# Optimization experiments

Hardware: AMD Instinct MI355X
Metric: run time of the kernel (lower is better)

The kernel has to match this reference:

```python
import jax, jax.numpy as jnp
import numpy as np

RX = (2, 9)
RY = (4, 9)
G, O = 64, 2          # column chunk size and overlap (hardcoded in original forward)
GK = RX[1]            # Gaussian (uniform box) kernel size, must be odd
M = N = 512


def _patches(x, kh, kw, pc, pr):
    # torch: F.pad(x,(pr,pr,pc,pc)).unfold(-2,kh,1).unfold(-2,kw,1).flatten(-2)
    xp = jnp.pad(x, ((0, 0), (0, 0), (pc, pc), (pr, pr)))
    p = jax.lax.conv_general_dilated_patches(xp, (kh, kw), (1, 1), 'VALID')  # (b, kh*kw, m, n) since c==1
    return jnp.moveaxis(p, 1, -1)[:, None]  # (b,1,m,n,kh*kw)


def _spatial_kernel(kh, kw):
    d = (jnp.arange(kh, dtype=jnp.float32) - kh // 2)[:, None] ** 2 \
        + (jnp.arange(kw, dtype=jnp.float32) - kw // 2)[None, :] ** 2
    return jnp.exp(-d.reshape(-1) / ((kh * kw) / 4.0) ** 2)


def _gen_weight(ych, kh, kw, pc, pr, sigma):
    p = _patches(ych, kh, kw, pc, pr)
    w = jnp.exp(-((p - ych[..., None]) ** 2) / (sigma / 2.0) ** 2)  # range (bilateral) term
    w = w * _spatial_kernel(kh, kw)                                  # spatial Gaussian term
    w = w * _patches(jnp.ones_like(ych), kh, kw, pc, pr)             # zero out padded taps
    return w / w.sum(-1, keepdims=True)


def _boxfilter(x, weight, kh, kw, pc, pr):
    return (_patches(x, kh, kw, pc, pr) * weight).sum(-1)


def _forward(X, y, r):
    sigma = r[0] * (y.max() - y.min())
    kh0, kw0, pc0, pr0 = 2 * RX[0] + 1, 2 * RY[0] + 1, RX[0], RY[0]  # detail kernel
    kh1, kw1, pc1, pr1 = 2 * RX[1] + 1, 2 * RY[1] + 1, RX[1], RY[1]  # base kernel
    gk = jnp.ones((1, 1, GK, GK), X.dtype) / float(GK * GK)
    pad = GK // 2
    conv = lambda z: jax.lax.conv_general_dilated(z, gk, (1, 1), [(pad, pad), (pad, pad)])

    # Angle = [0]: rotate(.,0,expand=True) and CenterCrop(m,n) are identities.
    XX, yy = X, y
    XXbase, yybase = conv(XX), conv(yy)
    XXdetail, yydetail = XX - XXbase, yy - yybase

    n = X.shape[-1]
    idx = np.arange(n)
    chunks = [idx[i:i + G] for i in range(0, n, G - O)]
    if len(chunks[-1]) <= 5:
        chunks[-2] = np.arange(chunks[-2][0], n)
        del chunks[-1]

    bdetail, Abase, bbase = [], [], []
    for index, ck in enumerate(chunks):
        s, e = int(ck[0]), int(ck[-1]) + 1
        Xb, Xd = XXbase[..., s:e], XXdetail[..., s:e]
        yb, yd = yybase[..., s:e], yydetail[..., s:e]
        wD = _gen_weight(Xd, kh0, kw0, pc0, pr0, sigma)
        wB = _gen_weight(Xb, kh1, kw1, pc1, pr1, sigma)
        lo = 0 if index == 0 else O // 2
        hi = None if index == len(chunks) - 1 else -(O // 2)
        bdetail.append(_boxfilter(yd - Xd, wD, kh0, kw0, pc0, pr0)[..., lo:hi])
        mean_y = _boxfilter(yb, wB, kh1, kw1, pc1, pr1)
        mean_x = _boxfilter(Xb, wB, kh1, kw1, pc1, pr1)
        var_x = _boxfilter(Xb * Xb, wB, kh1, kw1, pc1, pr1) - mean_x * mean_x
        cov_xy = _boxfilter(Xb * yb, wB, kh1, kw1, pc1, pr1) - mean_x * mean_y
        A = cov_xy / (var_x + 1e-6)
        b = mean_y - A * mean_x
        bbase.append(b[..., lo:hi])
        Abase.append(A[..., lo:hi])

    bdetail = jnp.concatenate(bdetail, -1)
    Abase = jnp.concatenate(Abase, -1)
    bbase = jnp.concatenate(bbase, -1)
    return Abase * XXbase + bbase + XXdetail + bdetail


def setup_inputs() -> dict:
    key = jax.random.key(0)
    k1, k2, k3 = jax.random.split(key, 3)
    X = jax.random.uniform(k1, (1, 1, M, N), dtype=jnp.float32)
    y = jax.random.uniform(k2, (1, 1, M, N), dtype=jnp.float32)
    r = jax.random.uniform(k3, (1,), dtype=jnp.float32)
    return {"X": X, "y": y, "r": r}


def reference(X, y, r):
    return _forward(X, y, r)
```

## Files before the change

kernel.cpp:

```cpp
#include <hip/hip_runtime.h>

#define W 512

__device__ __forceinline__ float fexp2(float x) {
#if __has_builtin(__builtin_amdgcn_exp2f)
    return __builtin_amdgcn_exp2f(x);
#else
    return __expf(x * 0.6931471805599453f);
#endif
}

__global__ __launch_bounds__(256) void k_minmax(const float* __restrict__ y,
                                                float2* __restrict__ partial) {
    __shared__ float smn[256], smx[256];
    int t = threadIdx.x;
    const float4* y4 = (const float4*)y;
    float4 v = y4[blockIdx.x * 256 + t];
    float mn = fminf(fminf(v.x, v.y), fminf(v.z, v.w));
    float mx = fmaxf(fmaxf(v.x, v.y), fmaxf(v.z, v.w));
    smn[t] = mn; smx[t] = mx;
    __syncthreads();
    for (int off = 128; off > 0; off >>= 1) {
        if (t < off) {
            smn[t] = fminf(smn[t], smn[t + off]);
            smx[t] = fmaxf(smx[t], smx[t + off]);
        }
        __syncthreads();
    }
    if (t == 0) partial[blockIdx.x] = make_float2(smn[0], smx[0]);
}

__global__ __launch_bounds__(256) void k_box(const float* __restrict__ X,
                                             const float* __restrict__ y,
                                             const float2* __restrict__ partial,
                                             const float* __restrict__ r,
                                             float2* __restrict__ bXY_g,
                                             float2* __restrict__ dXD_g,
                                             float* __restrict__ k2out) {
    __shared__ __align__(16) float lds[1920];
    float* sX  = lds;
    float* sY  = sX + 576;
    float* csX = sY + 576;
    float* csY = csX + 384;

    int tx = threadIdx.x, ty = threadIdx.y;
    int t = ty * 16 + tx;
    int c0 = blockIdx.x * 16, r0 = blockIdx.y * 16;

    if (blockIdx.x == 0 && blockIdx.y == 0) {
        float2* red = (float2*)lds;
        red[t] = partial[t];
        __syncthreads();
        for (int off = 128; off > 0; off >>= 1) {
            if (t < off) {
                red[t].x = fminf(red[t].x, red[t + off].x);
                red[t].y = fmaxf(red[t].y, red[t + off].y);
            }
            __syncthreads();
        }
        if (t == 0) {
            float sigma = r[0] * (red[0].y - red[0].x);
            float hh = 0.5f * sigma;
            k2out[0] = -1.4426950408889634f / (hh * hh);
        }
        __syncthreads();
    }

    for (int i = t; i < 576; i += 256) {
        int rr = i / 24, cc = i - rr * 24;
        int gr = r0 - 4 + rr, gc = c0 - 4 + cc;
        bool ok = ((unsigned)gr < 512u) & ((unsigned)gc < 512u);
        float xv = 0.f, yv = 0.f;
        if (ok) { xv = X[gr * W + gc]; yv = y[gr * W + gc]; }
        sX[i] = xv; sY[i] = yv;
    }
    __syncthreads();

    for (int i = t; i < 384; i += 256) {
        int rr = i / 24, cc = i - rr * 24;
        float ax = 0.f, ay = 0.f;
#pragma unroll
        for (int k = 0; k < 9; ++k) { ax += sX[(rr + k) * 24 + cc]; ay += sY[(rr + k) * 24 + cc]; }
        csX[i] = ax; csY[i] = ay;
    }
    __syncthreads();

    const float inv81 = 1.0f / 81.0f;
    float ax = 0.f, ay = 0.f;
#pragma unroll
    for (int k = 0; k < 9; ++k) { ax += csX[ty * 24 + tx + k]; ay += csY[ty * 24 + tx + k]; }
    float Xb = ax * inv81, yb = ay * inv81;
    float xc = sX[(ty + 4) * 24 + tx + 4];
    float yc = sY[(ty + 4) * 24 + tx + 4];
    float xd = xc - Xb;
    int p = (r0 + ty) * W + (c0 + tx);
    bXY_g[p] = make_float2(Xb, yb);
    dXD_g[p] = make_float2(xd, (yc - yb) - xd);
}

__global__ __launch_bounds__(256, 4) void k_bil(const float2* __restrict__ bXY_g,
                                                const float2* __restrict__ dXD_g,
                                                const float* __restrict__ k2buf,
                                                float* __restrict__ out) {
    __shared__ float sbx[19];
    __shared__ float sdy[5];
    __shared__ __align__(16) float2 bXYs[34 * 34];
    __shared__ __align__(16) float2 dXDs[20 * 24];

    int tx = threadIdx.x, ty = threadIdx.y;
    int t = ty * 16 + tx;
    int c0 = blockIdx.x * 16, r0 = blockIdx.y * 16;

    if (t < 19)      { int d = t - 9;  sbx[t]      = __expf(-(float)(d * d) / 8145.0625f); }
    else if (t < 24) { int d = t - 21; sdy[t - 19] = __expf(-(float)(d * d) / 126.5625f); }

    float k2 = k2buf[0];

    for (int i = t; i < 34 * 34; i += 256) {
        int rr = i / 34, cc2 = i - rr * 34;
        int gr = r0 - 9 + rr, gc = c0 - 9 + cc2;
        float2 v = make_float2(0.f, 0.f);
        if (((unsigned)gr < 512u) & ((unsigned)gc < 512u)) v = bXY_g[gr * W + gc];
        bXYs[i] = v;
    }
    for (int i = t; i < 20 * 24; i += 256) {
        int rr = i / 24, cc2 = i - rr * 24;
        int gr = r0 - 2 + rr, gc = c0 - 4 + cc2;
        float2 v = make_float2(0.f, 0.f);
        if (((unsigned)gr < 512u) & ((unsigned)gc < 512u)) v = dXD_g[gr * W + gc];
        dXDs[i] = v;
    }
    __syncthreads();

    int c = c0 + tx;
    int h = r0 + ty;

    int chunk = (c == 0) ? 0 : (c - 1) / 62;
    if (chunk > 8) chunk = 8;
    int s = 62 * chunk;
    int e = (chunk == 8) ? 512 : (s + 64);

    const float ksb = -1.4426950408889634f / 8145.0625f;
    const float ksd = -1.4426950408889634f / 126.5625f;
    float cc[19];
#pragma unroll
    for (int j = 0; j < 19; ++j) {
        int nc = c - 9 + j, d = j - 9;
        cc[j] = ((nc >= s) & (nc < e)) ? ksb * (float)(d * d) : -1e30f;
    }
    float ccd[9];
#pragma unroll
    for (int j = 0; j < 9; ++j) {
        int nc = c - 4 + j, d = j - 4;
        ccd[j] = ((nc >= s) & (nc < e)) ? ksd * (float)(d * d) : -1e30f;
    }

    float Xc = bXYs[(ty + 9) * 34 + tx + 9].x;
    float Xd = dXDs[(ty + 2) * 24 + tx + 4].x;

    float sw = 0.f, swx = 0.f, swy = 0.f, swxx = 0.f, swxy = 0.f;
#pragma unroll 1
    for (int k = 0; k < 19; ++k) {
        int nh = h - 9 + k;
        if ((unsigned)nh >= 512u) continue;
        const float2* xr = (const float2*)bXYs + (ty + k) * 34 + tx;
        float rs = 0.f, rsx = 0.f, rsy = 0.f, rsxx = 0.f, rsxy = 0.f;
#pragma unroll
        for (int j = 0; j < 19; ++j) {
            float2 v = xr[j];
            float u = v.x - Xc;
            float a = fmaf(u * k2, u, cc[j]);
            float w = fexp2(a);
            rs += w;
            rsx = fmaf(w, v.x, rsx);
            rsy = fmaf(w, v.y, rsy);
            float tt = w * v.x;
            rsxx = fmaf(tt, v.x, rsxx);
            rsxy = fmaf(tt, v.y, rsxy);
        }
        float ey = sbx[k];
        sw   = fmaf(ey, rs,   sw);
        swx  = fmaf(ey, rsx,  swx);
        swy  = fmaf(ey, rsy,  swy);
        swxx = fmaf(ey, rsxx, swxx);
        swxy = fmaf(ey, rsxy, swxy);
    }

    float swd = 0.f, sv = 0.f;
#pragma unroll 1
    for (int k = 0; k < 5; ++k) {
        int nh = h - 2 + k;
        if ((unsigned)nh >= 512u) continue;
        const float2* dr2 = (const float2*)dXDs + (ty + k) * 24 + tx;
        float rs = 0.f, rv = 0.f;
#pragma unroll
        for (int j = 0; j < 9; ++j) {
            float2 v = dr2[j];
            float u = v.x - Xd;
            float a = fmaf(u * k2, u, ccd[j]);
            float w = fexp2(a);
            rs += w;
            rv = fmaf(w, v.y, rv);
        }
        swd = fmaf(sdy[k], rs, swd);
        sv  = fmaf(sdy[k], rv, sv);
    }

    float inv  = 1.0f / sw;
    float mx   = swx * inv, my = swy * inv;
    float varx = fmaf(-mx, mx, swxx * inv);
    float cov  = fmaf(-mx, my, swxy * inv);
    float A    = cov / (varx + 1e-6f);
    float b    = my - A * mx;
    float bd   = sv / swd;
    out[h * W + c] = fmaf(A, Xc, b) + Xd + bd;
}

__global__ __launch_bounds__(256, 4) void k_fused(const float* __restrict__ X,
                                                  const float* __restrict__ y,
                                                  const float2* __restrict__ partial,
                                                  const float* __restrict__ r,
                                                  float* __restrict__ out) {
    __shared__ float sbx[19];
    __shared__ float sdy[5];
    __shared__ __align__(16) char ldsbuf[38624];
    float*  sX  = (float*)ldsbuf;
    float*  sY  = sX + 42 * 42;
    float*  csX = sY + 42 * 42;
    float*  csY = csX + 34 * 42;
    float2* bXY = (float2*)(csY + 34 * 42);
    float2* dXD = bXY + 34 * 34;
    float2* red = (float2*)sX;

    int tx = threadIdx.x, ty = threadIdx.y;
    int t = ty * 16 + tx;
    int c0 = blockIdx.x * 16, r0 = blockIdx.y * 16;

    if (t < 19)      { int d = t - 9;  sbx[t]      = __expf(-(float)(d * d) / 8145.0625f); }
    else if (t < 24) { int d = t - 21; sdy[t - 19] = __expf(-(float)(d * d) / 126.5625f); }

    red[t] = partial[t];
    __syncthreads();
    for (int off = 128; off > 0; off >>= 1) {
        if (t < off) {
            red[t].x = fminf(red[t].x, red[t + off].x);
            red[t].y = fmaxf(red[t].y, red[t + off].y);
        }
        __syncthreads();
    }
    float2 mm0 = red[0];
    __syncthreads();
    float sigma = r[0] * (mm0.y - mm0.x);
    float hh = 0.5f * sigma;
    float k2 = -1.4426950408889634f / (hh * hh);

    for (int i = t; i < 42 * 42; i += 256) {
        int rr = i / 42, cc2 = i - rr * 42;
        int gr = r0 - 13 + rr, gc = c0 - 13 + cc2;
        bool ok = ((unsigned)gr < 512u) & ((unsigned)gc < 512u);
        float xv = 0.f, yv = 0.f;
        if (ok) { xv = X[gr * W + gc]; yv = y[gr * W + gc]; }
        sX[i] = xv; sY[i] = yv;
    }
    __syncthreads();

    for (int i = t; i < 34 * 42; i += 256) {
        int rr = i / 42, cc2 = i - rr * 42;
        float ax = 0.f, ay = 0.f;
#pragma unroll
        for (int k = 0; k < 9; ++k) { ax += sX[(rr + k) * 42 + cc2]; ay += sY[(rr + k) * 42 + cc2]; }
        csX[i] = ax; csY[i] = ay;
    }
    __syncthreads();

    const float inv81 = 1.0f / 81.0f;
    for (int i = t; i < 34 * 34; i += 256) {
        int rr = i / 34, cc2 = i - rr * 34;
        float ax = 0.f, ay = 0.f;
#pragma unroll
        for (int k = 0; k < 9; ++k) { ax += csX[rr * 42 + cc2 + k]; ay += csY[rr * 42 + cc2 + k]; }
        bXY[i] = make_float2(ax * inv81, ay * inv81);
    }
    __syncthreads();

    for (int i = t; i < 20 * 24; i += 256) {
        int rr = i / 24, cc2 = i - rr * 24;
        float2 b2 = bXY[(rr + 7) * 34 + (cc2 + 5)];
        float xc = sX[(rr + 11) * 42 + (cc2 + 9)];
        float yc = sY[(rr + 11) * 42 + (cc2 + 9)];
        float xd = xc - b2.x;
        dXD[i] = make_float2(xd, (yc - b2.y) - xd);
    }
    __syncthreads();

    int c = c0 + tx;
    int h = r0 + ty;
    int chunk = (c == 0) ? 0 : (c - 1) / 62;
    if (chunk > 8) chunk = 8;
    int s = 62 * chunk;
    int e = (chunk == 8) ? 512 : (s + 64);

    const float ksb = -1.4426950408889634f / 8145.0625f;
    const float ksd = -1.4426950408889634f / 126.5625f;
    float cc[19];
#pragma unroll
    for (int j = 0; j < 19; ++j) {
        int nc = c - 9 + j, d = j - 9;
        cc[j] = ((nc >= s) & (nc < e)) ? ksb * (float)(d * d) : -1e30f;
    }
    float ccd[9];
#pragma unroll
    for (int j = 0; j < 9; ++j) {
        int nc = c - 4 + j, d = j - 4;
        ccd[j] = ((nc >= s) & (nc < e)) ? ksd * (float)(d * d) : -1e30f;
    }

    float Xc = bXY[(ty + 9) * 34 + tx + 9].x;
    float Xd = dXD[(ty + 2) * 24 + tx + 4].x;

    float sw = 0.f, swx = 0.f, swy = 0.f, swxx = 0.f, swxy = 0.f;
#pragma unroll 1
    for (int k = 0; k < 19; ++k) {
        int nh = h - 9 + k;
        if ((unsigned)nh >= 512u) continue;
        const float2* xr = bXY + (ty + k) * 34 + tx;
        float rs = 0.f, rsx = 0.f, rsy = 0.f, rsxx = 0.f, rsxy = 0.f;
#pragma unroll
        for (int j = 0; j < 19; ++j) {
            float2 v = xr[j];
            float u = v.x - Xc;
            float a = fmaf(u * k2, u, cc[j]);
            float w = fexp2(a);
            rs += w;
            rsx = fmaf(w, v.x, rsx);
            rsy = fmaf(w, v.y, rsy);
            float tt = w * v.x;
            rsxx = fmaf(tt, v.x, rsxx);
            rsxy = fmaf(tt, v.y, rsxy);
        }
        float ey = sbx[k];
        sw   = fmaf(ey, rs,   sw);
        swx  = fmaf(ey, rsx,  swx);
        swy  = fmaf(ey, rsy,  swy);
        swxx = fmaf(ey, rsxx, swxx);
        swxy = fmaf(ey, rsxy, swxy);
    }

    float swd = 0.f, sv = 0.f;
#pragma unroll 1
    for (int k = 0; k < 5; ++k) {
        int nh = h - 2 + k;
        if ((unsigned)nh >= 512u) continue;
        const float2* dr2 = dXD + (ty + k) * 24 + tx;
        float rs = 0.f, rv = 0.f;
#pragma unroll
        for (int j = 0; j < 9; ++j) {
            float2 v = dr2[j];
            float u = v.x - Xd;
            float a = fmaf(u * k2, u, ccd[j]);
            float w = fexp2(a);
            rs += w;
            rv = fmaf(w, v.y, rv);
        }
        swd = fmaf(sdy[k], rs, swd);
        sv  = fmaf(sdy[k], rv, sv);
    }

    float inv  = 1.0f / sw;
    float mx   = swx * inv, my = swy * inv;
    float varx = fmaf(-mx, mx, swxx * inv);
    float cov  = fmaf(-mx, my, swxy * inv);
    float A    = cov / (varx + 1e-6f);
    float b    = my - A * mx;
    float bd   = sv / swd;
    out[h * W + c] = fmaf(A, Xc, b) + Xd + bd;
}

extern "C" void kernel_launch(void* const* d_in, const int* in_sizes, int n_in,
                              void* d_out, int out_size, void* d_ws, size_t ws_size,
                              hipStream_t stream) {
    const float* X = (const float*)d_in[0];
    const float* y = (const float*)d_in[1];
    const float* r = (const float*)d_in[2];
    float* out = (float*)d_out;

    float2* partial = (float2*)d_ws;
    float*  k2buf   = (float*)((char*)d_ws + 2048);
    float2* bXY_g   = (float2*)((char*)d_ws + 4096);
    float2* dXD_g   = (float2*)((char*)d_ws + 4096 + 512 * 512 * 8);
    size_t need = 4096 + (size_t)2 * 512 * 512 * 8;

    k_minmax<<<256, 256, 0, stream>>>(y, partial);
    if (ws_size >= need) {
        k_box<<<dim3(32, 32), dim3(16, 16), 0, stream>>>(X, y, partial, r, bXY_g, dXD_g, k2buf);
        k_bil<<<dim3(32, 32), dim3(16, 16), 0, stream>>>(bXY_g, dXD_g, k2buf, out);
    } else {
        k_fused<<<dim3(32, 32), dim3(16, 16), 0, stream>>>(X, y, partial, r, out);
    }
}
```

Measured before the change: 96.23 us.

## Register-block bilateral kernel over four output rows per thread with 64x8 tiles

The bilateral kernel now computes four vertically adjacent output pixels per thread. Each shared-memory row of neighbours is loaded into registers once and reused across the four outputs, using shifted row-weight tables padded with zeros. Tiles change to 64 columns by 8 rows with 128-thread blocks, which cuts redundant halo loads and LDS reads per output. In exchange register pressure rises sharply (dozens of accumulators plus 38 cached values), occupancy drops, and there are fewer blocks in total (512).

```diff
diff --git a/kernel.cpp b/kernel.cpp
--- a/kernel.cpp
+++ b/kernel.cpp
@@ -98,33 +98,34 @@
     dXD_g[p] = make_float2(xd, (yc - yb) - xd);
 }
 
-__global__ __launch_bounds__(256, 4) void k_bil(const float2* __restrict__ bXY_g,
+__global__ __launch_bounds__(128, 1) void k_bil(const float2* __restrict__ bXY_g,
                                                 const float2* __restrict__ dXD_g,
                                                 const float* __restrict__ k2buf,
                                                 float* __restrict__ out) {
-    __shared__ float sbx[19];
-    __shared__ float sdy[5];
-    __shared__ __align__(16) float2 bXYs[34 * 34];
-    __shared__ __align__(16) float2 dXDs[20 * 24];
-
-    int tx = threadIdx.x, ty = threadIdx.y;
-    int t = ty * 16 + tx;
-    int c0 = blockIdx.x * 16, r0 = blockIdx.y * 16;
-
-    if (t < 19)      { int d = t - 9;  sbx[t]      = __expf(-(float)(d * d) / 8145.0625f); }
-    else if (t < 24) { int d = t - 21; sdy[t - 19] = __expf(-(float)(d * d) / 126.5625f); }
+    __shared__ float sbe[25];
+    __shared__ float sde[11];
+    __shared__ __align__(16) float2 bXYs[26 * 82];
+    __shared__ __align__(16) float2 dXDs[12 * 72];
+
+    int tx = threadIdx.x;
+    int ty = threadIdx.y;
+    int t = ty * 64 + tx;
+    int c0 = blockIdx.x * 64, r0 = blockIdx.y * 8;
+
+    if (t < 25)                 { int dy = t - 12; sbe[t] = (dy * dy <= 81) ? __expf(-(float)(dy * dy) / 8145.0625f) : 0.f; }
+    else if (t >= 32 && t < 43) { int i = t - 32; int dy = i - 5; sde[i] = (dy * dy <= 4) ? __expf(-(float)(dy * dy) / 126.5625f) : 0.f; }
 
     float k2 = k2buf[0];
 
-    for (int i = t; i < 34 * 34; i += 256) {
-        int rr = i / 34, cc2 = i - rr * 34;
+    for (int i = t; i < 26 * 82; i += 128) {
+        int rr = i / 82, cc2 = i - rr * 82;
         int gr = r0 - 9 + rr, gc = c0 - 9 + cc2;
         float2 v = make_float2(0.f, 0.f);
         if (((unsigned)gr < 512u) & ((unsigned)gc < 512u)) v = bXY_g[gr * W + gc];
         bXYs[i] = v;
     }
-    for (int i = t; i < 20 * 24; i += 256) {
-        int rr = i / 24, cc2 = i - rr * 24;
+    for (int i = t; i < 12 * 72; i += 128) {
+        int rr = i / 72, cc2 = i - rr * 72;
         int gr = r0 - 2 + rr, gc = c0 - 4 + cc2;
         float2 v = make_float2(0.f, 0.f);
         if (((unsigned)gr < 512u) & ((unsigned)gc < 512u)) v = dXD_g[gr * W + gc];
@@ -133,7 +134,7 @@
     __syncthreads();
 
     int c = c0 + tx;
-    int h = r0 + ty;
+    int h0 = r0 + 4 * ty;
 
     int chunk = (c == 0) ? 0 : (c - 1) / 62;
     if (chunk > 8) chunk = 8;
@@ -155,65 +156,98 @@
         ccd[j] = ((nc >= s) & (nc < e)) ? ksd * (float)(d * d) : -1e30f;
     }
 
-    float Xc = bXYs[(ty + 9) * 34 + tx + 9].x;
-    float Xd = dXDs[(ty + 2) * 24 + tx + 4].x;
-
-    float sw = 0.f, swx = 0.f, swy = 0.f, swxx = 0.f, swxy = 0.f;
+    float Xc[4], Xd[4];
+#pragma unroll
+    for (int p = 0; p < 4; ++p) {
+        Xc[p] = bXYs[(4 * ty + 9 + p) * 82 + tx + 9].x;
+        Xd[p] = dXDs[(4 * ty + 2 + p) * 72 + tx + 4].x;
+    }
+
+    float s_w[4], s_wx[4], s_wy[4], s_wxx[4], s_wxy[4];
+#pragma unroll
+    for (int p = 0; p < 4; ++p) { s_w[p] = 0.f; s_wx[p] = 0.f; s_wy[p] = 0.f; s_wxx[p] = 0.f; s_wxy[p] = 0.f; }
+
 #pragma unroll 1
-    for (int k = 0; k < 19; ++k) {
-        int nh = h - 9 + k;
-        if ((unsigned)nh >= 512u) continue;
-        const float2* xr = (const float2*)bXYs + (ty + k) * 34 + tx;
-        float rs = 0.f, rsx = 0.f, rsy = 0.f, rsxx = 0.f, rsxy = 0.f;
+    for (int k = 0; k < 22; ++k) {
+        int nh = h0 - 9 + k;
+        bool valid = (unsigned)nh < 512u;
+        const float2* xr = bXYs + (4 * ty + k) * 82 + tx;
+        float vx[19], vy[19];
+#pragma unroll
+        for (int j = 0; j < 19; ++j) { float2 v = xr[j]; vx[j] = v.x; vy[j] = v.y; }
+        float rs[4], rsx[4], rsy[4], rsxx[4], rsxy[4];
+#pragma unroll
+        for (int p = 0; p < 4; ++p) { rs[p] = 0.f; rsx[p] = 0.f; rsy[p] = 0.f; rsxx[p] = 0.f; rsxy[p] = 0.f; }
 #pragma unroll
         for (int j = 0; j < 19; ++j) {
-            float2 v = xr[j];
-            float u = v.x - Xc;
-            float a = fmaf(u * k2, u, cc[j]);
-            float w = fexp2(a);
-            rs += w;
-            rsx = fmaf(w, v.x, rsx);
-            rsy = fmaf(w, v.y, rsy);
-            float tt = w * v.x;
-            rsxx = fmaf(tt, v.x, rsxx);
-            rsxy = fmaf(tt, v.y, rsxy);
-        }
-        float ey = sbx[k];
-        sw   = fmaf(ey, rs,   sw);
-        swx  = fmaf(ey, rsx,  swx);
-        swy  = fmaf(ey, rsy,  swy);
-        swxx = fmaf(ey, rsxx, swxx);
-        swxy = fmaf(ey, rsxy, swxy);
-    }
-
-    float swd = 0.f, sv = 0.f;
+#pragma unroll
+            for (int p = 0; p < 4; ++p) {
+                float u = vx[j] - Xc[p];
+                float a = fmaf(u * k2, u, cc[j]);
+                float w = fexp2(a);
+                rs[p] += w;
+                rsx[p] = fmaf(w, vx[j], rsx[p]);
+                rsy[p] = fmaf(w, vy[j], rsy[p]);
+                float tt = w * vx[j];
+                rsxx[p] = fmaf(tt, vx[j], rsxx[p]);
+                rsxy[p] = fmaf(tt, vy[j], rsxy[p]);
+            }
+        }
+#pragma unroll
+        for (int p = 0; p < 4; ++p) {
+            float ey = valid ? sbe[k + 3 - p] : 0.f;
+            s_w[p]   = fmaf(ey, rs[p],   s_w[p]);
+            s_wx[p]  = fmaf(ey, rsx[p],  s_wx[p]);
+            s_wy[p]  = fmaf(ey, rsy[p],  s_wy[p]);
+            s_wxx[p] = fmaf(ey, rsxx[p], s_wxx[p]);
+            s_wxy[p] = fmaf(ey, rsxy[p], s_wxy[p]);
+        }
+    }
+
+    float s_wd[4], s_v[4];
+#pragma unroll
+    for (int p = 0; p < 4; ++p) { s_wd[p] = 0.f; s_v[p] = 0.f; }
 #pragma unroll 1
-    for (int k = 0; k < 5; ++k) {
-        int nh = h - 2 + k;
-        if ((unsigned)nh >= 512u) continue;
-        const float2* dr2 = (const float2*)dXDs + (ty + k) * 24 + tx;
-        float rs = 0.f, rv = 0.f;
+    for (int kd = 0; kd < 8; ++kd) {
+        int nh = h0 - 2 + kd;
+        bool valid = (unsigned)nh < 512u;
+        const float2* dr = dXDs + (4 * ty + kd) * 72 + tx;
+        float vx[9], vd[9];
+#pragma unroll
+        for (int j = 0; j < 9; ++j) { float2 v = dr[j]; vx[j] = v.x; vd[j] = v.y; }
+        float rs[4], rv[4];
+#pragma unroll
+        for (int p = 0; p < 4; ++p) { rs[p] = 0.f; rv[p] = 0.f; }
 #pragma unroll
         for (int j = 0; j < 9; ++j) {
-            float2 v = dr2[j];
-            float u = v.x - Xd;
-            float a = fmaf(u * k2, u, ccd[j]);
-            float w = fexp2(a);
-            rs += w;
-            rv = fmaf(w, v.y, rv);
-        }
-        swd = fmaf(sdy[k], rs, swd);
-        sv  = fmaf(sdy[k], rv, sv);
-    }
-
-    float inv  = 1.0f / sw;
-    float mx   = swx * inv, my = swy * inv;
-    float varx = fmaf(-mx, mx, swxx * inv);
-    float cov  = fmaf(-mx, my, swxy * inv);
-    float A    = cov / (varx + 1e-6f);
-    float b    = my - A * mx;
-    float bd   = sv / swd;
-    out[h * W + c] = fmaf(A, Xc, b) + Xd + bd;
+#pragma unroll
+            for (int p = 0; p < 4; ++p) {
+                float u = vx[j] - Xd[p];
+                float a = fmaf(u * k2, u, ccd[j]);
+                float w = fexp2(a);
+                rs[p] += w;
+                rv[p] = fmaf(w, vd[j], rv[p]);
+            }
+        }
+#pragma unroll
+        for (int p = 0; p < 4; ++p) {
+            float ey = valid ? sde[kd + 3 - p] : 0.f;
+            s_wd[p] = fmaf(ey, rs[p], s_wd[p]);
+            s_v[p]  = fmaf(ey, rv[p], s_v[p]);
+        }
+    }
+
+#pragma unroll
+    for (int p = 0; p < 4; ++p) {
+        float inv  = 1.0f / s_w[p];
+        float mx   = s_wx[p] * inv, my = s_wy[p] * inv;
+        float varx = fmaf(-mx, mx, s_wxx[p] * inv);
+        float cov  = fmaf(-mx, my, s_wxy[p] * inv);
+        float A    = cov / (varx + 1e-6f);
+        float b    = my - A * mx;
+        float bd   = s_v[p] / s_wd[p];
+        out[(h0 + p) * W + c] = fmaf(A, Xc[p], b) + Xd[p] + bd;
+    }
 }
 
 __global__ __launch_bounds__(256, 4) void k_fused(const float* __restrict__ X,
@@ -393,7 +427,7 @@
     k_minmax<<<256, 256, 0, stream>>>(y, partial);
     if (ws_size >= need) {
         k_box<<<dim3(32, 32), dim3(16, 16), 0, stream>>>(X, y, partial, r, bXY_g, dXD_g, k2buf);
-        k_bil<<<dim3(32, 32), dim3(16, 16), 0, stream>>>(bXY_g, dXD_g, k2buf, out);
+        k_bil<<<dim3(8, 64), dim3(64, 2), 0, stream>>>(bXY_g, dXD_g, k2buf, out);
     } else {
         k_fused<<<dim3(32, 32), dim3(16, 16), 0, stream>>>(X, y, partial, r, out);
     }
```

New measurement: 143.7 us. 1.49x slower.
